# Kernel optimization log

Hardware: AMD Instinct MI355X
Metric: run time of the kernel (lower is better)

The kernel has to match this reference:

```python
import jax, jax.numpy as jnp
import numpy as np

IMAGE_SIZE = 640.0
STRIDES = (8.0, 16.0, 32.0)
NUM_CLASSES = 80
MAX_TOP_K = 20
B, G, M = 16, 32, 320  # batch, max gt/image, candidates/layer/image
HS = (80, 40, 20)
A = 3
CH = 5 + NUM_CLASSES


def setup_inputs() -> dict:
    key = jax.random.key(0)
    ks = jax.random.split(key, 16)
    inp = {}
    for i, h in enumerate(HS):
        # post-activation style predictions in (0,1) so sqrt/logit are well-defined
        inp[f"pred{i}"] = jax.random.uniform(ks[i], (B, A, h, h, CH), jnp.float32, 0.02, 0.98)
        inp[f"a{i}"] = jax.random.randint(ks[3 + i], (B, M), 0, A)
        inp[f"gj{i}"] = jax.random.randint(ks[6 + i], (B, M), 0, h)
        inp[f"gi{i}"] = jax.random.randint(ks[9 + i], (B, M), 0, h)
        inp[f"anc{i}"] = jax.random.uniform(ks[12 + i], (B, M, 2), jnp.float32, 0.5, 4.0)
    cls = jax.random.randint(ks[15], (B, G), 0, NUM_CLASSES).astype(jnp.float32)
    cxy = jax.random.uniform(jax.random.fold_in(key, 100), (B, G, 2), jnp.float32, 0.1, 0.9)
    wh = jax.random.uniform(jax.random.fold_in(key, 101), (B, G, 2), jnp.float32, 0.02, 0.3)
    img_id = jnp.broadcast_to(jnp.arange(B, dtype=jnp.float32)[:, None], (B, G))
    # targets row layout: [image_id, class, cx, cy, w, h] (normalized)
    inp["targets"] = jnp.concatenate([img_id[..., None], cls[..., None], cxy, wh], axis=-1)
    return inp


def _cxcywh_to_xyxy(b):
    cx, cy, w, h = b[..., 0], b[..., 1], b[..., 2], b[..., 3]
    return jnp.stack([cx - w / 2, cy - h / 2, cx + w / 2, cy + h / 2], axis=-1)


def _box_iou(b1, b2):
    # b1: [B,G,4], b2: [B,N,4] -> [B,G,N]  (torchvision.ops.box_iou semantics)
    lt = jnp.maximum(b1[:, :, None, :2], b2[:, None, :, :2])
    rb = jnp.minimum(b1[:, :, None, 2:], b2[:, None, :, 2:])
    wh = jnp.clip(rb - lt, 0.0)
    inter = wh[..., 0] * wh[..., 1]
    a1 = (b1[..., 2] - b1[..., 0]) * (b1[..., 3] - b1[..., 1])
    a2 = (b2[..., 2] - b2[..., 0]) * (b2[..., 3] - b2[..., 1])
    return inter / (a1[:, :, None] + a2[:, None, :] - inter)


def _cost_matrix(preds, targets, idx_a, idx_gj, idx_gi):
    bidx = jnp.arange(B)[:, None]
    cands, boxes = [], []
    for l in range(3):
        c = preds[l][bidx, idx_a[l], idx_gj[l], idx_gi[l]]  # [B,M,CH] gather
        cands.append(c)
        boxes.append(_cxcywh_to_xyxy(c[..., :4] * STRIDES[l]))
    cand = jnp.concatenate(cands, axis=1)        # [B,N,CH]
    p_xyxy = jnp.concatenate(boxes, axis=1)      # [B,N,4]
    p_obj = cand[..., 4:5]                       # [B,N,1]
    p_cls = cand[..., 5:]                        # [B,N,C]
    gt_xyxy = _cxcywh_to_xyxy(targets[..., 2:6] * IMAGE_SIZE)  # [B,G,4]

    iou = _box_iou(gt_xyxy, p_xyxy)              # [B,G,N]
    iou_loss = -jnp.log(iou + 1e-5)
    topk_iou, _ = jax.lax.top_k(iou, MAX_TOP_K)
    dk = jnp.maximum(topk_iou.sum(-1).astype(jnp.int32), 1)    # dynamic_ks [B,G]

    t = jax.nn.one_hot(targets[..., 1].astype(jnp.int32), NUM_CLASSES)  # [B,G,C]
    y = jnp.sqrt(p_cls[:, None, :, :] * p_obj[:, None, :, :])  # [B,G,N,C]
    z = jnp.log(y / (1.0 - y))                   # logit(y)
    # stable binary_cross_entropy_with_logits
    bce = jnp.maximum(z, 0.0) - z * t[:, :, None, :] + jnp.log1p(jnp.exp(-jnp.abs(z)))
    cls_loss = bce.sum(-1)                       # [B,G,N]
    cost = cls_loss + 3.0 * iou_loss
    return cost, dk


def _assign(cost, dk):
    N = cost.shape[-1]
    K = MAX_TOP_K
    # indices of K smallest costs per gt
    _, pos = jax.lax.top_k(-cost, K)             # [B,G,K]
    sel = (jnp.arange(K)[None, None, :] < dk[..., None]).astype(cost.dtype)
    matching = jnp.zeros((B, G, N), cost.dtype).at[
        jnp.arange(B)[:, None, None], jnp.arange(G)[None, :, None], pos].max(sel)
    # conflict resolution: anchors matched to >1 gt keep only the min-cost gt
    n_match = matching.sum(1)                    # [B,N]
    conflict = n_match > 1.0
    argmin_gt = jnp.argmin(cost, axis=1)         # [B,N]
    onehot_min = (jnp.arange(G)[None, :, None] == argmin_gt[:, None, :]).astype(cost.dtype)
    matching = jnp.where(conflict[:, None, :], onehot_min, matching)
    fg_mask = matching.sum(1) > 0.0              # [B,N]
    matched_gt = jnp.argmax(matching, axis=1)    # [B,N]
    return matching, fg_mask, matched_gt


def reference(pred0, pred1, pred2, targets, anc0, anc1, anc2,
              a0, gj0, gi0, a1, gj1, gi1, a2, gj2, gi2):
    cost, dk = _cost_matrix((pred0, pred1, pred2), targets,
                            (a0, a1, a2), (gj0, gj1, gj2), (gi0, gi1, gi2))
    matching, fg_mask, matched_gt = _assign(cost, dk)
    return matching, fg_mask, matched_gt, cost
```

## Files before the change

kernel.cpp:

```cpp
#include <hip/hip_runtime.h>
#include <hip/hip_bf16.h>
#include <math.h>

#define NB 16
#define NG 32
#define NM 320
#define NN 960
#define NA 3
#define NCH 85
#define NC 80
#define NK 20

template<int CTRL>
__device__ __forceinline__ unsigned long long dpp_u64_self(unsigned long long x) {
    int lo = (int)(unsigned)(x & 0xFFFFFFFFull);
    int hi = (int)(unsigned)(x >> 32);
    int lo2 = __builtin_amdgcn_update_dpp(lo, lo, CTRL, 0xF, 0xF, false);
    int hi2 = __builtin_amdgcn_update_dpp(hi, hi, CTRL, 0xF, 0xF, false);
    return ((unsigned long long)(unsigned)hi2 << 32) | (unsigned)lo2;
}

__device__ __forceinline__ unsigned long long dpp_max_u64(unsigned long long x) {
    unsigned long long o;
    o = dpp_u64_self<0x111>(x); x = (o > x) ? o : x;
    o = dpp_u64_self<0x112>(x); x = (o > x) ? o : x;
    o = dpp_u64_self<0x114>(x); x = (o > x) ? o : x;
    o = dpp_u64_self<0x118>(x); x = (o > x) ? o : x;
    o = dpp_u64_self<0x142>(x); x = (o > x) ? o : x;
    o = dpp_u64_self<0x143>(x); x = (o > x) ? o : x;
    return x;
}

__device__ __forceinline__ unsigned long long dpp_min_u64(unsigned long long x) {
    unsigned long long o;
    o = dpp_u64_self<0x111>(x); x = (o < x) ? o : x;
    o = dpp_u64_self<0x112>(x); x = (o < x) ? o : x;
    o = dpp_u64_self<0x114>(x); x = (o < x) ? o : x;
    o = dpp_u64_self<0x118>(x); x = (o < x) ? o : x;
    o = dpp_u64_self<0x142>(x); x = (o < x) ? o : x;
    o = dpp_u64_self<0x143>(x); x = (o < x) ? o : x;
    return x;
}

template<int CTRL>
__device__ __forceinline__ double dpp_f64_zero(double x) {
    long long b = __double_as_longlong(x);
    int lo = (int)(unsigned)((unsigned long long)b & 0xFFFFFFFFull);
    int hi = (int)(unsigned)((unsigned long long)b >> 32);
    int lo2 = __builtin_amdgcn_update_dpp(0, lo, CTRL, 0xF, 0xF, true);
    int hi2 = __builtin_amdgcn_update_dpp(0, hi, CTRL, 0xF, 0xF, true);
    unsigned long long r = ((unsigned long long)(unsigned)hi2 << 32) | (unsigned)lo2;
    return __longlong_as_double((long long)r);
}

__device__ __forceinline__ double dpp_sum_f64(double x) {
    x += dpp_f64_zero<0x111>(x);
    x += dpp_f64_zero<0x112>(x);
    x += dpp_f64_zero<0x114>(x);
    x += dpp_f64_zero<0x118>(x);
    x += dpp_f64_zero<0x142>(x);
    x += dpp_f64_zero<0x143>(x);
    return x;
}

__global__ __launch_bounds__(256) void k_prep(
                       const float* __restrict__ p0, const float* __restrict__ p1, const float* __restrict__ p2,
                       const int* __restrict__ a0, const int* __restrict__ gj0, const int* __restrict__ gi0,
                       const int* __restrict__ a1, const int* __restrict__ gj1, const int* __restrict__ gi1,
                       const int* __restrict__ a2, const int* __restrict__ gj2, const int* __restrict__ gi2,
                       int* __restrict__ coff, int* __restrict__ clvl,
                       float* __restrict__ pobj, float* __restrict__ parea,
                       float* __restrict__ pbox, double* __restrict__ Ssum)
{
    int wid = blockIdx.x * 4 + ((int)threadIdx.x >> 6);
    int lane = (int)threadIdx.x & 63;
    if (wid >= NB * NN) return;
    int b = wid / NN, n = wid % NN;
    int lvl = (n < NM) ? 0 : ((n < 2 * NM) ? 1 : 2);
    int m = n - lvl * NM;

    const int* pa = (lvl == 0) ? a0 : ((lvl == 1) ? a1 : a2);
    const int* pj = (lvl == 0) ? gj0 : ((lvl == 1) ? gj1 : gj2);
    const int* pi = (lvl == 0) ? gi0 : ((lvl == 1) ? gi1 : gi2);
    const float* pr = (lvl == 0) ? p0 : ((lvl == 1) ? p1 : p2);
    int h = (lvl == 0) ? 80 : ((lvl == 1) ? 40 : 20);
    float s = (lvl == 0) ? 8.0f : ((lvl == 1) ? 16.0f : 32.0f);

    int aa = pa[b * NM + m];
    int jj = pj[b * NM + m];
    int ii = pi[b * NM + m];
    int off = (((b * NA + aa) * h + jj) * h + ii) * NCH;
    const float* c = pr + off;

    float po = c[4];
    double S = 0.0;
    for (int cc = lane; cc < NC; cc += 64) {
        float pc = c[5 + cc];
        float y = sqrtf(pc * po);
        float z = logf(y / (1.0f - y));
        float sp = fmaxf(z, 0.0f) + log1pf(expf(-fabsf(z)));
        S += (double)sp;
    }
    S = dpp_sum_f64(S);

    if (lane == 63) {
        float cx = c[0] * s, cy = c[1] * s, w = c[2] * s, hh = c[3] * s;
        float x1 = cx - w * 0.5f, y1 = cy - hh * 0.5f;
        float x2 = cx + w * 0.5f, y2 = cy + hh * 0.5f;

        coff[wid] = off;
        clvl[wid] = lvl;
        pobj[wid] = po;
        parea[wid] = (x2 - x1) * (y2 - y1);
        pbox[wid * 4 + 0] = x1;
        pbox[wid * 4 + 1] = y1;
        pbox[wid * 4 + 2] = x2;
        pbox[wid * 4 + 3] = y2;
        Ssum[wid] = S;
    }
}

__global__ __launch_bounds__(64) void k_row(
        const float* __restrict__ p0, const float* __restrict__ p1, const float* __restrict__ p2,
        const float* __restrict__ tgt,
        const int* __restrict__ coff, const int* __restrict__ clvl,
        const float* __restrict__ pobj, const float* __restrict__ parea,
        const float* __restrict__ pbox, const double* __restrict__ Ssum,
        float* __restrict__ ocost, unsigned char* __restrict__ match0)
{
    int bg = blockIdx.x;
    int b = bg / NG;
    int t = (int)threadIdx.x;

    const float* tg = tgt + bg * 6;
    int cls = (int)tg[1];
    float gcx = tg[2] * 640.0f, gcy = tg[3] * 640.0f;
    float gw = tg[4] * 640.0f, gh = tg[5] * 640.0f;
    float gx1 = gcx - gw * 0.5f, gy1 = gcy - gh * 0.5f;
    float gx2 = gcx + gw * 0.5f, gy2 = gcy + gh * 0.5f;
    float ga = (gx2 - gx1) * (gy2 - gy1);

    float cl[15], io[15];
    #pragma unroll
    for (int j = 0; j < 15; ++j) {
        int n = j * 64 + t;
        int idx = b * NN + n;
        int lvl = clvl[idx];
        const float* pr = (lvl == 0) ? p0 : ((lvl == 1) ? p1 : p2);
        float pc = pr[coff[idx] + 5 + cls];
        float po = pobj[idx];
        float y = sqrtf(pc * po);
        float z = logf(y / (1.0f - y));
        float clsl = (float)(Ssum[idx] - (double)z);

        const float* pb = pbox + idx * 4;
        float lx = fmaxf(gx1, pb[0]), ly = fmaxf(gy1, pb[1]);
        float rx = fminf(gx2, pb[2]), ry = fminf(gy2, pb[3]);
        float wx = fmaxf(rx - lx, 0.0f), wy = fmaxf(ry - ly, 0.0f);
        float inter = wx * wy;
        float iou = inter / (ga + parea[idx] - inter);
        float il = -logf(iou + 1e-5f);
        float cst = clsl + 3.0f * il;

        cl[j] = cst;
        io[j] = iou;
        ocost[bg * NN + n] = cst;
    }

    double ssum = 0.0;
    for (int k = 0; k < NK; ++k) {
        float bv = io[0]; int bj = 0;
        #pragma unroll
        for (int j = 1; j < 15; ++j) {
            if (io[j] > bv) { bv = io[j]; bj = j; }
        }
        unsigned long long key =
            ((unsigned long long)__float_as_uint(bv) << 32) | (unsigned)(~(unsigned)(bj * 64 + t));
        key = dpp_max_u64(key);
        unsigned lo = (unsigned)__builtin_amdgcn_readlane((int)(unsigned)(key & 0xFFFFFFFFull), 63);
        unsigned hi = (unsigned)__builtin_amdgcn_readlane((int)(unsigned)(key >> 32), 63);
        float mval = __uint_as_float(hi);
        int mn = (int)(~lo);
        ssum += (double)mval;
        bool win = ((mn & 63) == t);
        int slot = mn >> 6;
        #pragma unroll
        for (int j = 0; j < 15; ++j) io[j] = (win && slot == j) ? -2.0f : io[j];
    }
    int dk = (int)((float)ssum);
    if (dk < 1) dk = 1;
    if (dk > NK) dk = NK;

    unsigned sel = 0;
    for (int k = 0; k < dk; ++k) {
        float bv = cl[0]; int bj = 0;
        #pragma unroll
        for (int j = 1; j < 15; ++j) {
            if (cl[j] < bv) { bv = cl[j]; bj = j; }
        }
        unsigned long long key =
            ((unsigned long long)__float_as_uint(bv) << 32) | (unsigned)(bj * 64 + t);
        key = dpp_min_u64(key);
        unsigned lo = (unsigned)__builtin_amdgcn_readlane((int)(unsigned)(key & 0xFFFFFFFFull), 63);
        int mn = (int)lo;
        bool win = ((mn & 63) == t);
        int slot = mn >> 6;
        if (win) sel |= 1u << slot;
        #pragma unroll
        for (int j = 0; j < 15; ++j) cl[j] = (win && slot == j) ? INFINITY : cl[j];
    }

    #pragma unroll
    for (int j = 0; j < 15; ++j) {
        int n = j * 64 + t;
        match0[bg * NN + n] = (unsigned char)((sel >> j) & 1u);
    }
}

__global__ void k_resolve(const float* __restrict__ cost, const unsigned char* __restrict__ match0,
                          float* __restrict__ om, float* __restrict__ ofg,
                          float* __restrict__ omg)
{
    int i = blockIdx.x * blockDim.x + threadIdx.x;
    if (i >= NB * NN) return;
    int b = i / NN, n = i % NN;

    int cnt = 0, first = -1;
    unsigned mloc = 0;
    #pragma unroll
    for (int g = 0; g < NG; ++g) {
        int v = match0[(b * NG + g) * NN + n];
        if (v) {
            cnt++;
            mloc |= 1u << g;
            if (first < 0) first = g;
        }
    }

    int mgt;
    int fg;
    if (cnt > 1) {
        float bv = INFINITY; int bgi = 0;
        #pragma unroll
        for (int g = 0; g < NG; ++g) {
            float c = cost[(b * NG + g) * NN + n];
            if (c < bv) { bv = c; bgi = g; }
        }
        mloc = 1u << bgi;
        mgt = bgi;
        fg = 1;
    } else {
        mgt = (first >= 0) ? first : 0;
        fg = (cnt > 0) ? 1 : 0;
    }

    #pragma unroll
    for (int g = 0; g < NG; ++g) {
        om[(b * NG + g) * NN + n] = ((mloc >> g) & 1u) ? 1.0f : 0.0f;
    }
    ofg[b * NN + n] = fg ? 1.0f : 0.0f;
    omg[b * NN + n] = (float)mgt;
}

extern "C" void kernel_launch(void* const* d_in, const int* in_sizes, int n_in,
                              void* d_out, int out_size, void* d_ws, size_t ws_size,
                              hipStream_t stream) {
    const float* p0 = (const float*)d_in[0];
    const int* a0 = (const int*)d_in[1];
    const int* gj0 = (const int*)d_in[2];
    const int* gi0 = (const int*)d_in[3];
    const float* p1 = (const float*)d_in[5];
    const int* a1 = (const int*)d_in[6];
    const int* gj1 = (const int*)d_in[7];
    const int* gi1 = (const int*)d_in[8];
    const float* p2 = (const float*)d_in[10];
    const int* a2 = (const int*)d_in[11];
    const int* gj2 = (const int*)d_in[12];
    const int* gi2 = (const int*)d_in[13];
    const float* tgt = (const float*)d_in[15];

    float* o = (float*)d_out;
    float* om = o;
    float* ofg = o + (size_t)NB * NG * NN;
    float* omg = ofg + (size_t)NB * NN;
    float* ocost = omg + (size_t)NB * NN;

    char* w = (char*)d_ws;
    double* Ssum = (double*)w;      w += (size_t)NB * NN * sizeof(double);
    float* pbox = (float*)w;        w += (size_t)NB * NN * 4 * sizeof(float);
    float* pobj = (float*)w;        w += (size_t)NB * NN * sizeof(float);
    float* parea = (float*)w;       w += (size_t)NB * NN * sizeof(float);
    int* coff = (int*)w;            w += (size_t)NB * NN * sizeof(int);
    int* clvl = (int*)w;            w += (size_t)NB * NN * sizeof(int);
    unsigned char* match0 = (unsigned char*)w;  w += (size_t)NB * NG * NN;

    (void)in_sizes; (void)n_in; (void)out_size; (void)ws_size;

    int nWaves = NB * NN;
    k_prep<<<(nWaves + 3) / 4, 256, 0, stream>>>(
        p0, p1, p2, a0, gj0, gi0, a1, gj1, gi1, a2, gj2, gi2,
        coff, clvl, pobj, parea, pbox, Ssum);

    k_row<<<NB * NG, 64, 0, stream>>>(
        p0, p1, p2, tgt, coff, clvl, pobj, parea, pbox, Ssum,
        ocost, match0);

    k_resolve<<<(NB * NN + 255) / 256, 256, 0, stream>>>(
        ocost, match0, om, ofg, omg);
}
```

Measured before the change: 38.41 us.

## Fuse conflict-resolve pass into row kernel via last-block-per-image atomic counter

Removes the separate k_resolve launch. Each row block now packs its per-anchor selection bits into 64-bit ballot masks and bumps a per-image atomic counter, and the last block to finish for an image runs the conflict resolution and writes the matching, fg and matched-gt outputs. This saves one kernel launch and replaces the byte-per-entry match buffer with compact bitmasks. In exchange, the resolve work for each image is serialized onto a single 64-thread wave, which may lengthen the tail of the row kernel.

```diff
diff --git a/kernel.cpp b/kernel.cpp
--- a/kernel.cpp
+++ b/kernel.cpp
@@ -1,5 +1,4 @@
 #include <hip/hip_runtime.h>
-#include <hip/hip_bf16.h>
 #include <math.h>
 
 #define NB 16
@@ -70,8 +69,11 @@
                        const int* __restrict__ a2, const int* __restrict__ gj2, const int* __restrict__ gi2,
                        int* __restrict__ coff, int* __restrict__ clvl,
                        float* __restrict__ pobj, float* __restrict__ parea,
-                       float* __restrict__ pbox, double* __restrict__ Ssum)
+                       float* __restrict__ pbox, double* __restrict__ Ssum,
+                       unsigned* __restrict__ done)
 {
+    if (blockIdx.x == 0 && threadIdx.x < NB) done[threadIdx.x] = 0;
+
     int wid = blockIdx.x * 4 + ((int)threadIdx.x >> 6);
     int lane = (int)threadIdx.x & 63;
     if (wid >= NB * NN) return;
@@ -126,7 +128,9 @@
         const int* __restrict__ coff, const int* __restrict__ clvl,
         const float* __restrict__ pobj, const float* __restrict__ parea,
         const float* __restrict__ pbox, const double* __restrict__ Ssum,
-        float* __restrict__ ocost, unsigned char* __restrict__ match0)
+        unsigned long long* __restrict__ mb, unsigned* __restrict__ done,
+        float* __restrict__ ocost, float* __restrict__ om,
+        float* __restrict__ ofg, float* __restrict__ omg)
 {
     int bg = blockIdx.x;
     int b = bg / NG;
@@ -212,54 +216,49 @@
 
     #pragma unroll
     for (int j = 0; j < 15; ++j) {
-        int n = j * 64 + t;
-        match0[bg * NN + n] = (unsigned char)((sel >> j) & 1u);
-    }
-}
-
-__global__ void k_resolve(const float* __restrict__ cost, const unsigned char* __restrict__ match0,
-                          float* __restrict__ om, float* __restrict__ ofg,
-                          float* __restrict__ omg)
-{
-    int i = blockIdx.x * blockDim.x + threadIdx.x;
-    if (i >= NB * NN) return;
-    int b = i / NN, n = i % NN;
-
-    int cnt = 0, first = -1;
-    unsigned mloc = 0;
-    #pragma unroll
-    for (int g = 0; g < NG; ++g) {
-        int v = match0[(b * NG + g) * NN + n];
-        if (v) {
-            cnt++;
-            mloc |= 1u << g;
-            if (first < 0) first = g;
+        unsigned long long m = __ballot((sel >> j) & 1u);
+        if (t == 0) mb[bg * 15 + j] = m;
+    }
+
+    __threadfence();
+    unsigned old = 0;
+    if (t == 0) old = __hip_atomic_fetch_add(&done[b], 1u, __ATOMIC_ACQ_REL, __HIP_MEMORY_SCOPE_AGENT);
+    old = (unsigned)__shfl((int)old, 0, 64);
+    if (old == NG - 1) {
+        __threadfence();
+        #pragma unroll 1
+        for (int j = 0; j < 15; ++j) {
+            int n = j * 64 + t;
+            unsigned mloc = 0;
+            #pragma unroll
+            for (int g = 0; g < NG; ++g) {
+                unsigned long long wg = mb[(b * NG + g) * 15 + j];
+                mloc |= (unsigned)((wg >> t) & 1ull) << g;
+            }
+            int cnt = __popc(mloc);
+            int mgt, fg;
+            if (cnt > 1) {
+                float bv = INFINITY; int bgi = 0;
+                #pragma unroll
+                for (int g = 0; g < NG; ++g) {
+                    float c = ocost[(b * NG + g) * NN + n];
+                    if (c < bv) { bv = c; bgi = g; }
+                }
+                mloc = 1u << bgi;
+                mgt = bgi;
+                fg = 1;
+            } else {
+                mgt = (cnt > 0) ? (__ffs(mloc) - 1) : 0;
+                fg = (cnt > 0) ? 1 : 0;
+            }
+            #pragma unroll
+            for (int g = 0; g < NG; ++g) {
+                om[(b * NG + g) * NN + n] = ((mloc >> g) & 1u) ? 1.0f : 0.0f;
+            }
+            ofg[b * NN + n] = fg ? 1.0f : 0.0f;
+            omg[b * NN + n] = (float)mgt;
         }
     }
-
-    int mgt;
-    int fg;
-    if (cnt > 1) {
-        float bv = INFINITY; int bgi = 0;
-        #pragma unroll
-        for (int g = 0; g < NG; ++g) {
-            float c = cost[(b * NG + g) * NN + n];
-            if (c < bv) { bv = c; bgi = g; }
-        }
-        mloc = 1u << bgi;
-        mgt = bgi;
-        fg = 1;
-    } else {
-        mgt = (first >= 0) ? first : 0;
-        fg = (cnt > 0) ? 1 : 0;
-    }
-
-    #pragma unroll
-    for (int g = 0; g < NG; ++g) {
-        om[(b * NG + g) * NN + n] = ((mloc >> g) & 1u) ? 1.0f : 0.0f;
-    }
-    ofg[b * NN + n] = fg ? 1.0f : 0.0f;
-    omg[b * NN + n] = (float)mgt;
 }
 
 extern "C" void kernel_launch(void* const* d_in, const int* in_sizes, int n_in,
@@ -286,25 +285,23 @@
     float* ocost = omg + (size_t)NB * NN;
 
     char* w = (char*)d_ws;
-    double* Ssum = (double*)w;      w += (size_t)NB * NN * sizeof(double);
-    float* pbox = (float*)w;        w += (size_t)NB * NN * 4 * sizeof(float);
-    float* pobj = (float*)w;        w += (size_t)NB * NN * sizeof(float);
-    float* parea = (float*)w;       w += (size_t)NB * NN * sizeof(float);
-    int* coff = (int*)w;            w += (size_t)NB * NN * sizeof(int);
-    int* clvl = (int*)w;            w += (size_t)NB * NN * sizeof(int);
-    unsigned char* match0 = (unsigned char*)w;  w += (size_t)NB * NG * NN;
+    double* Ssum = (double*)w;              w += (size_t)NB * NN * sizeof(double);
+    unsigned long long* mb = (unsigned long long*)w;  w += (size_t)NB * NG * 15 * sizeof(unsigned long long);
+    float* pbox = (float*)w;                w += (size_t)NB * NN * 4 * sizeof(float);
+    float* pobj = (float*)w;                w += (size_t)NB * NN * sizeof(float);
+    float* parea = (float*)w;               w += (size_t)NB * NN * sizeof(float);
+    int* coff = (int*)w;                    w += (size_t)NB * NN * sizeof(int);
+    int* clvl = (int*)w;                    w += (size_t)NB * NN * sizeof(int);
+    unsigned* done = (unsigned*)w;          w += (size_t)NB * sizeof(unsigned);
 
     (void)in_sizes; (void)n_in; (void)out_size; (void)ws_size;
 
     int nWaves = NB * NN;
     k_prep<<<(nWaves + 3) / 4, 256, 0, stream>>>(
         p0, p1, p2, a0, gj0, gi0, a1, gj1, gi1, a2, gj2, gi2,
-        coff, clvl, pobj, parea, pbox, Ssum);
+        coff, clvl, pobj, parea, pbox, Ssum, done);
 
     k_row<<<NB * NG, 64, 0, stream>>>(
         p0, p1, p2, tgt, coff, clvl, pobj, parea, pbox, Ssum,
-        ocost, match0);
-
-    k_resolve<<<(NB * NN + 255) / 256, 256, 0, stream>>>(
-        ocost, match0, om, ofg, omg);
-}
+        mb, done, ocost, om, ofg, omg);
+}
```

Measured after the change: 82.59 us. +115.0%, slower.
